# Optimization experiments

Hardware: AMD Instinct MI355X
Metric: run time of the kernel (lower is better)

Reference implementation:

```python
import jax, jax.numpy as jnp
import numpy as np

N, T, D, H = 64, 512, 512, 1024


def setup_inputs() -> dict:
    key = jax.random.key(0)
    k1, k2, k3, k4 = jax.random.split(key, 4)
    x = jax.random.normal(k1, (N, T, D), dtype=jnp.float32)
    h0 = jax.random.normal(k2, (N, H), dtype=jnp.float32)
    Wx = jax.random.normal(k3, (D, H), dtype=jnp.float32) / jnp.sqrt(jnp.float32(D))
    Wh = jax.random.normal(k4, (H, H), dtype=jnp.float32) / jnp.sqrt(jnp.float32(H))
    b = jnp.zeros((H,), dtype=jnp.float32)
    return {"x": x, "h0": h0, "Wx": Wx, "Wh": Wh, "b": b}


def reference(x, h0, Wx, Wh, b):
    # Precompute input-to-hidden projections for all timesteps in one big GEMM:
    # (N, T, D) @ (D, H) -> (N, T, H). Mathematically identical to per-step x_t @ Wx.
    xw = jnp.einsum("ntd,dh->nth", x, Wx) + b  # (N, T, H)

    def step(h_prev, xw_t):
        h_next = jnp.tanh(xw_t + h_prev @ Wh)  # (N, H)
        return h_next, h_next

    # scan over time: xw transposed to (T, N, H)
    _, h_seq = jax.lax.scan(step, h0, jnp.swapaxes(xw, 0, 1))
    return jnp.swapaxes(h_seq, 0, 1)  # (N, T, H)
```

## Files before the change

### kernel.cpp

```cpp
#include <hip/hip_runtime.h>


#define NN 64
#define TT 512
#define DD 512
#define HH 1024

typedef unsigned int  u32;
typedef unsigned short u16;

typedef __attribute__((ext_vector_type(8))) short bf16x8;
typedef __attribute__((ext_vector_type(4))) float f32x4;
typedef __attribute__((ext_vector_type(4))) u32   u32x4;
typedef __attribute__((ext_vector_type(2))) u32   u32x2;

#define MFMA16(a, b, c) __builtin_amdgcn_mfma_f32_16x16x32_bf16((a), (b), (c), 0, 0, 0)

__device__ __forceinline__ u32 bf16r(float f) {
    u32 u = __float_as_uint(f);
    return (u + 0x7fffu + ((u >> 16) & 1u)) >> 16;
}
__device__ __forceinline__ float bf16tof(u32 h) { return __uint_as_float(h << 16); }
__device__ __forceinline__ void split2(float f, u32& hi, u32& lo) {
    hi = bf16r(f);
    lo = bf16r(f - bf16tof(hi));
}

__device__ __forceinline__ u32x4 ld16_sys(const u32* p) {
    u32x4 v;
    asm volatile("global_load_dwordx4 %0, %1, off sc0 sc1" : "=&v"(v) : "v"(p));
    return v;
}
__device__ __forceinline__ void st8_sys(u32* p, u32 v0, u32 v1) {
    u32x2 v = {v0, v1};
    asm volatile("global_store_dwordx2 %0, %1, off sc0 sc1" :: "v"(p), "v"(v));
}
__device__ __forceinline__ void st_flag(u32* p, u32 v) {
    asm volatile("global_store_dword %0, %1, off sc0 sc1" :: "v"(p), "v"(v));
}
__device__ __forceinline__ void wait_vm0() {
    asm volatile("s_waitcnt vmcnt(0)");
}

__device__ __forceinline__ float fast_tanh(float x) {
    float e = __expf(2.0f * x);
    return 1.0f - __fdividef(2.0f, e + 1.0f);
}

__global__ __launch_bounds__(256) void prep_kernel(
    const float* __restrict__ Wx, const float* __restrict__ Wh,
    const float* __restrict__ h0,
    u16* __restrict__ WxPh, u16* __restrict__ WxPl,
    u16* __restrict__ WhPh, u16* __restrict__ WhPl,
    u32* __restrict__ hpk)
{
    const int stride = gridDim.x * 256;
    const int gid = blockIdx.x * 256 + threadIdx.x;

    for (int p = gid; p < 64 * 16 * 64 * 8; p += stride) {
        int e = p & 7, l = (p >> 3) & 63, kb = (p >> 9) & 15, jt = p >> 13;
        int j = jt * 16 + (l & 15);
        int k = kb * 32 + ((l >> 4) << 3) + e;
        u32 hi, lo; split2(Wx[k * HH + j], hi, lo);
        WxPh[p] = (u16)hi; WxPl[p] = (u16)lo;
    }
    for (int p = gid; p < 64 * 32 * 64 * 8; p += stride) {
        int e = p & 7, l = (p >> 3) & 63, kb = (p >> 9) & 31, jt = p >> 14;
        int j = jt * 16 + (l & 15);
        int k = kb * 32 + ((l >> 4) << 3) + e;
        u32 hi, lo; split2(Wh[k * HH + j], hi, lo);
        WhPh[p] = (u16)hi; WhPl[p] = (u16)lo;
    }
    for (int p = gid; p < NN * HH; p += stride) {
        u32 hi, lo; split2(h0[p], hi, lo);
        int n = p >> 10, j = p & 1023;
        int gg = n >> 4, row = n & 15;
        int kb = j >> 5, c = j & 31;
        int lane_f = row | (((c >> 3) & 3) << 4);
        int e = c & 7;
        hpk[((4 + gg) * 32 + kb) * 512 + lane_f * 8 + e] = (hi << 16) | lo;
    }
}

__global__ __launch_bounds__(256) void gemm_kernel(
    const float* __restrict__ x, const float* __restrict__ b,
    const u16* __restrict__ WxPh, const u16* __restrict__ WxPl,
    float* __restrict__ out)
{
    __shared__ __align__(16) u32 ldsA[2][128][20];

    const int tid = threadIdx.x;
    const int bid = blockIdx.x;
    const int w   = tid >> 6;
    const int l   = tid & 63;
    const int wm = w >> 1, wj = w & 1;

    const int m0 = (bid >> 3) * 128;
    const int jb = bid & 7;
    const int j0 = jb * 128;

    f32x4 acc[4][4] = {};
    for (int ks = 0; ks < 16; ++ks) {
        const int k0 = ks * 32;
        #pragma unroll
        for (int it = 0; it < 8; ++it) {
            int idx = it * 256 + tid;
            int m = idx >> 4, kp = idx & 15;
            float2 v = *(const float2*)(x + (m0 + m) * DD + k0 + kp * 2);
            u32 h0b, l0b, h1b, l1b;
            split2(v.x, h0b, l0b);
            split2(v.y, h1b, l1b);
            ldsA[0][m][kp] = h0b | (h1b << 16);
            ldsA[1][m][kp] = l0b | (l1b << 16);
        }
        __syncthreads();

        bf16x8 afh[4], afl[4], bfh[4], bfl[4];
        #pragma unroll
        for (int mt4 = 0; mt4 < 4; ++mt4) {
            int row = wm * 64 + mt4 * 16 + (l & 15);
            int co  = (l >> 4) * 4;
            afh[mt4] = *(const bf16x8*)&ldsA[0][row][co];
            afl[mt4] = *(const bf16x8*)&ldsA[1][row][co];
        }
        #pragma unroll
        for (int jt4 = 0; jt4 < 4; ++jt4) {
            int jtile = jb * 8 + wj * 4 + jt4;
            int off = ((jtile * 16 + ks) * 64 + l) * 8;
            bfh[jt4] = *(const bf16x8*)(WxPh + off);
            bfl[jt4] = *(const bf16x8*)(WxPl + off);
        }
        #pragma unroll
        for (int mt4 = 0; mt4 < 4; ++mt4)
            #pragma unroll
            for (int jt4 = 0; jt4 < 4; ++jt4) {
                acc[mt4][jt4] = MFMA16(afh[mt4], bfh[jt4], acc[mt4][jt4]);
                acc[mt4][jt4] = MFMA16(afh[mt4], bfl[jt4], acc[mt4][jt4]);
                acc[mt4][jt4] = MFMA16(afl[mt4], bfh[jt4], acc[mt4][jt4]);
            }
        __syncthreads();
    }
    #pragma unroll
    for (int jt4 = 0; jt4 < 4; ++jt4) {
        int j = j0 + wj * 64 + jt4 * 16 + (l & 15);
        float bj = b[j];
        #pragma unroll
        for (int mt4 = 0; mt4 < 4; ++mt4)
            #pragma unroll
            for (int r = 0; r < 4; ++r) {
                int m = m0 + wm * 64 + mt4 * 16 + (l >> 4) * 4 + r;
                out[m * HH + j] = acc[mt4][jt4][r] + bj;
            }
    }
}

__global__ __launch_bounds__(256, 1) void scan_kernel(
    const u16* __restrict__ WhPh, const u16* __restrict__ WhPl,
    u32* __restrict__ hbuf,
    float* __restrict__ out, u32* __restrict__ flags)
{
    __shared__ __align__(16) char ldsWhH[65536];
    __shared__ __align__(16) char ldsWhL[65536];
    __shared__ float ldsRed[2][4][16][34];

    const int tid = threadIdx.x;
    const int bid = blockIdx.x;
    const int g   = bid & 3;
    const int cb  = bid >> 2;
    const int w   = tid >> 6;
    const int l   = tid & 63;

    for (int c = tid; c < 4096; c += 256) {
        int f = c >> 6, q = c & 63;
        int fw = f >> 4, fj = (f >> 3) & 1, fi = f & 7;
        int src = (((cb * 2 + fj) * 32) + (fw * 8 + fi)) * 512 + q * 8;
        *(u32x4*)(ldsWhH + c * 16) = *(const u32x4*)(WhPh + src);
        *(u32x4*)(ldsWhL + c * 16) = *(const u32x4*)(WhPl + src);
    }
    __syncthreads();

    const int rF = tid >> 4;
    const int nF = g * 16 + rF;
    const int c0 = (tid & 15) * 2;
    const int jE = cb * 32 + c0;

    const int lane_f = rF | (((c0 >> 3) & 3) << 4);
    const int eP     = c0 & 7;
    const int pOff   = (g * 32 + cb) * 512 + lane_f * 8 + eP;

    const int cOff   = (g * 32 + w * 8) * 512 + l * 8;

    u32* gf = flags + g * 512;
    u32* fp0 = gf + l * 4;
    u32* fp1 = gf + (l + 64) * 4;

    float2 xw = *(const float2*)&out[(nF * TT) * HH + jE];

    for (int t = 0; t < TT; ++t) {
        u32x4 bh[2][8], bl[2][8];
        #pragma unroll
        for (int jj = 0; jj < 2; ++jj)
            #pragma unroll
            for (int i = 0; i < 8; ++i) {
                int off = (((w * 2 + jj) * 8 + i) << 10) + (l << 4);
                bh[jj][i] = *(const u32x4*)(ldsWhH + off);
                bl[jj][i] = *(const u32x4*)(ldsWhL + off);
            }
        __builtin_amdgcn_sched_barrier(0);

        if (t > 0) {
            const u32 tgt = (u32)t;
            while (true) {
                u32 f0, f1;
                asm volatile("global_load_dword %0, %2, off sc0 sc1\n\t"
                             "global_load_dword %1, %3, off sc0 sc1\n\t"
                             "s_waitcnt vmcnt(0)"
                             : "=&v"(f0), "=&v"(f1) : "v"(fp0), "v"(fp1));
                if (__ballot((f0 >= tgt) && (f1 >= tgt)) == ~0ull) break;
            }
        }
        __builtin_amdgcn_sched_barrier(0);

        const u32* hp = hbuf + ((t - 1) & 1) * 4 * 32 * 512 + cOff;
        u32x4 a0[8], a1[8];
        #pragma unroll
        for (int i = 0; i < 8; ++i) {
            a0[i] = ld16_sys(hp + i * 512);
            a1[i] = ld16_sys(hp + i * 512 + 4);
        }
        wait_vm0();
        __builtin_amdgcn_sched_barrier(0);
        #pragma unroll
        for (int i = 0; i < 8; ++i) {
            asm volatile("" : "+v"(a0[i]));
            asm volatile("" : "+v"(a1[i]));
        }

        f32x4 ahh[2] = {}, ahl[2] = {}, alh[2] = {};
        #pragma unroll
        for (int i = 0; i < 8; ++i) {
            bf16x8 Ah, Al;
            #pragma unroll
            for (int e = 0; e < 4; ++e) {
                u32 u0 = a0[i][e], u1 = a1[i][e];
                Ah[e]     = (short)(u0 >> 16);
                Al[e]     = (short)(u0 & 0xFFFFu);
                Ah[4 + e] = (short)(u1 >> 16);
                Al[4 + e] = (short)(u1 & 0xFFFFu);
            }
            #pragma unroll
            for (int jj = 0; jj < 2; ++jj) {
                bf16x8 Bh = __builtin_bit_cast(bf16x8, bh[jj][i]);
                bf16x8 Bl = __builtin_bit_cast(bf16x8, bl[jj][i]);
                ahh[jj] = MFMA16(Ah, Bh, ahh[jj]);
                ahl[jj] = MFMA16(Ah, Bl, ahl[jj]);
                alh[jj] = MFMA16(Al, Bh, alh[jj]);
            }
        }

        const int par = t & 1;
        {
            int rb = (l >> 4) * 4, cc = l & 15;
            #pragma unroll
            for (int jj = 0; jj < 2; ++jj) {
                f32x4 s4 = ahh[jj] + ahl[jj] + alh[jj];
                #pragma unroll
                for (int e = 0; e < 4; ++e)
                    ldsRed[par][w][rb + e][jj * 16 + cc] = s4[e];
            }
        }
        __syncthreads();

        float sx = 0.f, sy = 0.f;
        #pragma unroll
        for (int wq = 0; wq < 4; ++wq) {
            float2 v = *(const float2*)&ldsRed[par][wq][rF][c0];
            sx += v.x; sy += v.y;
        }
        float hv0 = fast_tanh(xw.x + sx);
        float hv1 = fast_tanh(xw.y + sy);

        if (t + 1 < TT) {
            u32 hb0, lb0, hb1, lb1;
            split2(hv0, hb0, lb0);
            split2(hv1, hb1, lb1);
            st8_sys(hbuf + par * 4 * 32 * 512 + pOff,
                    (hb0 << 16) | lb0, (hb1 << 16) | lb1);
            wait_vm0();
            if (l == 0) st_flag(gf + (cb * 4 + w) * 4, (u32)(t + 1));
        }
        *(float2*)&out[(nF * TT + t) * HH + jE] = make_float2(hv0, hv1);
        if (t + 1 < TT)
            xw = *(const float2*)&out[(nF * TT + t + 1) * HH + jE];
    }
}

extern "C" void kernel_launch(void* const* d_in, const int* in_sizes, int n_in,
                              void* d_out, int out_size, void* d_ws, size_t ws_size,
                              hipStream_t stream) {
    const float* x  = (const float*)d_in[0];
    const float* h0 = (const float*)d_in[1];
    const float* Wx = (const float*)d_in[2];
    const float* Wh = (const float*)d_in[3];
    const float* b  = (const float*)d_in[4];
    float* out = (float*)d_out;

    char* ws = (char*)d_ws;
    u16* WxPh = (u16*)(ws);
    u16* WxPl = (u16*)(ws + (1u << 20));
    u16* WhPh = (u16*)(ws + (2u << 20));
    u16* WhPl = (u16*)(ws + (4u << 20));
    u32* hbuf = (u32*)(ws + (6u << 20));
    u32* flags= (u32*)(ws + (6u << 20) + (1u << 19));

    hipMemsetAsync(flags, 0, 4 * 512 * sizeof(u32), stream);
    prep_kernel<<<2048, 256, 0, stream>>>(Wx, Wh, h0, WxPh, WxPl, WhPh, WhPl, hbuf);
    gemm_kernel<<<2048, 256, 0, stream>>>(x, b, WxPh, WxPl, out);
    scan_kernel<<<128, 256, 0, stream>>>(WhPh, WhPl, hbuf, out, flags);
}
```

Baseline: 1.558 ms.

## Replace per-step flag polling with parity tags embedded in hidden-state data

Drops the separate flag array and its store-wait-flag handshake. Each packed hidden value now carries a parity tag in the lowest bit of its low bf16 half, so consumers poll the data itself and re-load only the chunks that are still stale. Loads for the next step are issued right after the store, which overlaps them with the output write. This removes one global round trip per step, but costs one bit of precision in the low correction term and relies on the 8-byte stores being observed atomically.

```diff
diff --git a/kernel.cpp b/kernel.cpp
--- a/kernel.cpp
+++ b/kernel.cpp
@@ -34,9 +34,6 @@
 __device__ __forceinline__ void st8_sys(u32* p, u32 v0, u32 v1) {
     u32x2 v = {v0, v1};
     asm volatile("global_store_dwordx2 %0, %1, off sc0 sc1" :: "v"(p), "v"(v));
-}
-__device__ __forceinline__ void st_flag(u32* p, u32 v) {
-    asm volatile("global_store_dword %0, %1, off sc0 sc1" :: "v"(p), "v"(v));
 }
 __device__ __forceinline__ void wait_vm0() {
     asm volatile("s_waitcnt vmcnt(0)");
@@ -78,7 +75,9 @@
         int kb = j >> 5, c = j & 31;
         int lane_f = row | (((c >> 3) & 3) << 4);
         int e = c & 7;
-        hpk[((4 + gg) * 32 + kb) * 512 + lane_f * 8 + e] = (hi << 16) | lo;
+        int slot = (gg * 32 + kb) * 512 + lane_f * 8 + e;
+        hpk[4 * 32 * 512 + slot] = (hi << 16) | (lo & 0xFFFEu) | 1u;
+        hpk[slot] = 1u;
     }
 }
 
@@ -157,7 +156,7 @@
 __global__ __launch_bounds__(256, 1) void scan_kernel(
     const u16* __restrict__ WhPh, const u16* __restrict__ WhPl,
     u32* __restrict__ hbuf,
-    float* __restrict__ out, u32* __restrict__ flags)
+    float* __restrict__ out)
 {
     __shared__ __align__(16) char ldsWhH[65536];
     __shared__ __align__(16) char ldsWhL[65536];
@@ -190,11 +189,17 @@
 
     const int cOff   = (g * 32 + w * 8) * 512 + l * 8;
 
-    u32* gf = flags + g * 512;
-    u32* fp0 = gf + l * 4;
-    u32* fp1 = gf + (l + 64) * 4;
-
     float2 xw = *(const float2*)&out[(nF * TT) * HH + jE];
+
+    u32x4 a0[8], a1[8];
+    {
+        const u32* hp = hbuf + 1 * 4 * 32 * 512 + cOff;
+        #pragma unroll
+        for (int i = 0; i < 8; ++i) {
+            a0[i] = ld16_sys(hp + i * 512);
+            a1[i] = ld16_sys(hp + i * 512 + 4);
+        }
+    }
 
     for (int t = 0; t < TT; ++t) {
         u32x4 bh[2][8], bl[2][8];
@@ -208,33 +213,36 @@
             }
         __builtin_amdgcn_sched_barrier(0);
 
-        if (t > 0) {
-            const u32 tgt = (u32)t;
-            while (true) {
-                u32 f0, f1;
-                asm volatile("global_load_dword %0, %2, off sc0 sc1\n\t"
-                             "global_load_dword %1, %3, off sc0 sc1\n\t"
-                             "s_waitcnt vmcnt(0)"
-                             : "=&v"(f0), "=&v"(f1) : "v"(fp0), "v"(fp1));
-                if (__ballot((f0 >= tgt) && (f1 >= tgt)) == ~0ull) break;
+        const u32 tgm = (u32)(((t - 1) >> 1) & 1);
+        const u32* hp = hbuf + ((t - 1) & 1) * 4 * 32 * 512 + cOff;
+
+        u32 pend = 0xFFu;
+        while (true) {
+            wait_vm0();
+            __builtin_amdgcn_sched_barrier(0);
+            #pragma unroll
+            for (int i = 0; i < 8; ++i)
+                asm volatile("" : "+v"(a0[i]), "+v"(a1[i]));
+            #pragma unroll
+            for (int i = 0; i < 8; ++i) {
+                if (pend & (1u << i)) {
+                    u32 bad = ((a0[i][0] ^ tgm) | (a0[i][1] ^ tgm)
+                             | (a0[i][2] ^ tgm) | (a0[i][3] ^ tgm)
+                             | (a1[i][0] ^ tgm) | (a1[i][1] ^ tgm)
+                             | (a1[i][2] ^ tgm) | (a1[i][3] ^ tgm)) & 1u;
+                    if (bad == 0u) pend &= ~(1u << i);
+                }
+            }
+            if (__ballot(pend != 0u) == 0ull) break;
+            #pragma unroll
+            for (int i = 0; i < 8; ++i) {
+                if (pend & (1u << i)) {
+                    a0[i] = ld16_sys(hp + i * 512);
+                    a1[i] = ld16_sys(hp + i * 512 + 4);
+                }
             }
         }
         __builtin_amdgcn_sched_barrier(0);
-
-        const u32* hp = hbuf + ((t - 1) & 1) * 4 * 32 * 512 + cOff;
-        u32x4 a0[8], a1[8];
-        #pragma unroll
-        for (int i = 0; i < 8; ++i) {
-            a0[i] = ld16_sys(hp + i * 512);
-            a1[i] = ld16_sys(hp + i * 512 + 4);
-        }
-        wait_vm0();
-        __builtin_amdgcn_sched_barrier(0);
-        #pragma unroll
-        for (int i = 0; i < 8; ++i) {
-            asm volatile("" : "+v"(a0[i]));
-            asm volatile("" : "+v"(a1[i]));
-        }
 
         f32x4 ahh[2] = {}, ahl[2] = {}, alh[2] = {};
         #pragma unroll
@@ -244,9 +252,9 @@
             for (int e = 0; e < 4; ++e) {
                 u32 u0 = a0[i][e], u1 = a1[i][e];
                 Ah[e]     = (short)(u0 >> 16);
-                Al[e]     = (short)(u0 & 0xFFFFu);
+                Al[e]     = (short)(u0 & 0xFFFEu);
                 Ah[4 + e] = (short)(u1 >> 16);
-                Al[4 + e] = (short)(u1 & 0xFFFFu);
+                Al[4 + e] = (short)(u1 & 0xFFFEu);
             }
             #pragma unroll
             for (int jj = 0; jj < 2; ++jj) {
@@ -281,13 +289,19 @@
         float hv1 = fast_tanh(xw.y + sy);
 
         if (t + 1 < TT) {
+            const u32 tagw = (u32)((t >> 1) & 1);
             u32 hb0, lb0, hb1, lb1;
             split2(hv0, hb0, lb0);
             split2(hv1, hb1, lb1);
             st8_sys(hbuf + par * 4 * 32 * 512 + pOff,
-                    (hb0 << 16) | lb0, (hb1 << 16) | lb1);
-            wait_vm0();
-            if (l == 0) st_flag(gf + (cb * 4 + w) * 4, (u32)(t + 1));
+                    (hb0 << 16) | (lb0 & 0xFFFEu) | tagw,
+                    (hb1 << 16) | (lb1 & 0xFFFEu) | tagw);
+            const u32* hpn = hbuf + par * 4 * 32 * 512 + cOff;
+            #pragma unroll
+            for (int i = 0; i < 8; ++i) {
+                a0[i] = ld16_sys(hpn + i * 512);
+                a1[i] = ld16_sys(hpn + i * 512 + 4);
+            }
         }
         *(float2*)&out[(nF * TT + t) * HH + jE] = make_float2(hv0, hv1);
         if (t + 1 < TT)
@@ -311,10 +325,8 @@
     u16* WhPh = (u16*)(ws + (2u << 20));
     u16* WhPl = (u16*)(ws + (4u << 20));
     u32* hbuf = (u32*)(ws + (6u << 20));
-    u32* flags= (u32*)(ws + (6u << 20) + (1u << 19));
-
-    hipMemsetAsync(flags, 0, 4 * 512 * sizeof(u32), stream);
+
     prep_kernel<<<2048, 256, 0, stream>>>(Wx, Wh, h0, WxPh, WxPl, WhPh, WhPl, hbuf);
     gemm_kernel<<<2048, 256, 0, stream>>>(x, b, WxPh, WxPl, out);
-    scan_kernel<<<128, 256, 0, stream>>>(WhPh, WhPl, hbuf, out, flags);
-}
+    scan_kernel<<<128, 256, 0, stream>>>(WhPh, WhPl, hbuf, out);
+}
```

Result: slower. 2.219 ms (+42.4%).

## Split cross-block flag wait into data-ready and write-after-read checks with prefetched flags

Applied to the files above, without the earlier changes.

Replaces the per-step poll of two flags per lane with two separate checks. One is a data-dependency flag check that is issued speculatively right after publishing the previous step. The other is a write-after-read check on the double-buffered h that is deferred until just before the next store. The aim is to take the flag polling latency off the critical path and overlap it with the h loads and MFMA work. The cost is more complex synchronisation logic, with some risk of ordering or visibility bugs in the cross-workgroup protocol.

```diff
diff --git a/kernel.cpp b/kernel.cpp
--- a/kernel.cpp
+++ b/kernel.cpp
@@ -190,11 +190,12 @@
 
     const int cOff   = (g * 32 + w * 8) * 512 + l * 8;
 
-    u32* gf = flags + g * 512;
-    u32* fp0 = gf + l * 4;
-    u32* fp1 = gf + (l + 64) * 4;
+    u32* gf  = flags + g * 512;
+    u32* fpD = gf + (32 * w + l) * 4;
+    u32* fpW = gf + (l * 4 + (cb >> 3)) * 4;
 
     float2 xw = *(const float2*)&out[(nF * TT) * HH + jE];
+    u32 fD = 0;
 
     for (int t = 0; t < TT; ++t) {
         u32x4 bh[2][8], bl[2][8];
@@ -211,17 +212,23 @@
         if (t > 0) {
             const u32 tgt = (u32)t;
             while (true) {
-                u32 f0, f1;
-                asm volatile("global_load_dword %0, %2, off sc0 sc1\n\t"
-                             "global_load_dword %1, %3, off sc0 sc1\n\t"
-                             "s_waitcnt vmcnt(0)"
-                             : "=&v"(f0), "=&v"(f1) : "v"(fp0), "v"(fp1));
-                if (__ballot((f0 >= tgt) && (f1 >= tgt)) == ~0ull) break;
+                wait_vm0();
+                __builtin_amdgcn_sched_barrier(0);
+                asm volatile("" : "+v"(fD));
+                bool ok = (l >= 32) || (fD >= tgt);
+                if (__ballot(ok) == ~0ull) break;
+                if (l < 32)
+                    asm volatile("global_load_dword %0, %1, off sc0 sc1"
+                                 : "=&v"(fD) : "v"(fpD));
             }
         }
         __builtin_amdgcn_sched_barrier(0);
 
         const u32* hp = hbuf + ((t - 1) & 1) * 4 * 32 * 512 + cOff;
+        u32 fW = 0xFFFFFFFFu;
+        if (l < 32)
+            asm volatile("global_load_dword %0, %1, off sc0 sc1"
+                         : "=&v"(fW) : "v"(fpW));
         u32x4 a0[8], a1[8];
         #pragma unroll
         for (int i = 0; i < 8; ++i) {
@@ -232,9 +239,9 @@
         __builtin_amdgcn_sched_barrier(0);
         #pragma unroll
         for (int i = 0; i < 8; ++i) {
-            asm volatile("" : "+v"(a0[i]));
-            asm volatile("" : "+v"(a1[i]));
-        }
+            asm volatile("" : "+v"(a0[i]), "+v"(a1[i]));
+        }
+        asm volatile("" : "+v"(fW));
 
         f32x4 ahh[2] = {}, ahl[2] = {}, alh[2] = {};
         #pragma unroll
@@ -281,6 +288,19 @@
         float hv1 = fast_tanh(xw.y + sy);
 
         if (t + 1 < TT) {
+            {
+                const u32 tgt = (u32)t;
+                while (true) {
+                    bool ok = (l >= 32) || (fW >= tgt);
+                    if (__ballot(ok) == ~0ull) break;
+                    if (l < 32)
+                        asm volatile("global_load_dword %0, %1, off sc0 sc1\n\t"
+                                     "s_waitcnt vmcnt(0)"
+                                     : "=&v"(fW) : "v"(fpW));
+                    __builtin_amdgcn_sched_barrier(0);
+                    asm volatile("" : "+v"(fW));
+                }
+            }
             u32 hb0, lb0, hb1, lb1;
             split2(hv0, hb0, lb0);
             split2(hv1, hb1, lb1);
@@ -288,6 +308,9 @@
                     (hb0 << 16) | lb0, (hb1 << 16) | lb1);
             wait_vm0();
             if (l == 0) st_flag(gf + (cb * 4 + w) * 4, (u32)(t + 1));
+            if (l < 32)
+                asm volatile("global_load_dword %0, %1, off sc0 sc1"
+                             : "=&v"(fD) : "v"(fpD));
         }
         *(float2*)&out[(nF * TT + t) * HH + jE] = make_float2(hv0, hv1);
         if (t + 1 < TT)
```

New measurement: 2.016 ms. 1.29x slower.
